# Kernel tuning notes

Measured on AMD Instinct MI355X. Metric: run time of the kernel, lower is better.

Reference implementation:

```python
import jax, jax.numpy as jnp
import numpy as np

SIZE = 1024
M = 10            # log2(SIZE); number of butterfly factors
N_TERMS = 10
BATCH = 8192

# diagonal offset of butterfly j (order matches torch: range(m)[::-1])
DIAGS = [1 << (M - 1 - j) for j in range(M)]


def setup_inputs() -> dict:
    key = jax.random.key(0)
    k1, k2, k3, k4, k5 = jax.random.split(key, 5)
    x = jax.random.normal(k1, (BATCH, SIZE), dtype=jnp.float32)
    diag = jax.random.normal(k2, (M, SIZE), dtype=jnp.float32)
    subpad = jax.random.normal(k3, (M, SIZE), dtype=jnp.float32)
    suppad = jax.random.normal(k4, (M, SIZE), dtype=jnp.float32)
    logit = jax.random.normal(k5, (N_TERMS, M), dtype=jnp.float32)
    # zero the padded positions: subdiag has length SIZE-d stored in [d:],
    # superdiag has length SIZE-d stored in [:-d]
    idx = np.arange(SIZE)
    sub_mask = np.stack([idx >= d for d in DIAGS]).astype(np.float32)
    sup_mask = np.stack([idx < SIZE - d for d in DIAGS]).astype(np.float32)
    subpad = subpad * jnp.asarray(sub_mask)
    suppad = suppad * jnp.asarray(sup_mask)
    return {"x": x, "diag": diag, "subpad": subpad, "suppad": suppad, "logit": logit}


def _butterfly(x, dg, sb, sp, d):
    # out = dg*x; out[d:] += subdiag*x[:-d]; out[:-d] += superdiag*x[d:]
    z = jnp.zeros(x.shape[:-1] + (d,), x.dtype)
    x_right = jnp.concatenate([z, x[..., :-d]], axis=-1)  # x shifted right by d
    x_left = jnp.concatenate([x[..., d:], z], axis=-1)    # x shifted left by d
    return dg * x + sb * x_right + sp * x_left


def reference(x, diag, subpad, suppad, logit):
    prob = jax.nn.softmax(logit, axis=-1)  # (n_terms, m)
    out = x
    for i in range(N_TERMS)[::-1]:
        # apply all m butterflies to current output, stack on last dim
        ys = jnp.stack(
            [_butterfly(out, diag[j], subpad[j], suppad[j], DIAGS[j]) for j in range(M)],
            axis=-1,
        )  # (..., size, m)
        out = jnp.einsum('bsm,m->bs', ys, prob[i])
    return out
```

## Files before the change

kernel.cpp:

```cpp
#include <hip/hip_runtime.h>

#define SIZE 1024
#define MM 10
#define NTERMS 10

typedef _Float16 f16;
typedef __attribute__((ext_vector_type(8))) _Float16 f16x8;
typedef __attribute__((ext_vector_type(4))) _Float16 f16x4;
typedef __attribute__((ext_vector_type(4))) float    f32x4;
typedef __attribute__((ext_vector_type(2))) int      i2;

typedef const __attribute__((address_space(1))) _Float16 gf16;
typedef __attribute__((address_space(3))) _Float16 sf16;

__device__ __forceinline__ float4 ldq(const float* p) { return *(const float4*)p; }

#define FMA4F(W, v0, v1, v2, v3)                                     \
    a0 = fmaf((W)[0], (v0), a0); a1 = fmaf((W)[1], (v1), a1);        \
    a2 = fmaf((W)[2], (v2), a2); a3 = fmaf((W)[3], (v3), a3);

__device__ __forceinline__ void cvt16(const float4& v0, const float4& v1, f16x8& h) {
    h[0] = (f16)v0.x; h[1] = (f16)v0.y; h[2] = (f16)v0.z; h[3] = (f16)v0.w;
    h[4] = (f16)v1.x; h[5] = (f16)v1.y; h[6] = (f16)v1.z; h[7] = (f16)v1.w;
}

__global__ __launch_bounds__(256)
void cvt_x(const float* __restrict__ x, f16* __restrict__ xh)
{
    const long i = ((long)blockIdx.x * 256 + threadIdx.x) * 16;
    const float4 a = ldq(x + i), b = ldq(x + i + 4),
                 c = ldq(x + i + 8), d = ldq(x + i + 12);
    f16x8 h0, h1; cvt16(a, b, h0); cvt16(c, d, h1);
    *(f16x8*)(xh + i)     = h0;
    *(f16x8*)(xh + i + 8) = h1;
}

__global__ __launch_bounds__(256, 2)
void precompute_G(const float* __restrict__ diag,
                  const float* __restrict__ subpad,
                  const float* __restrict__ suppad,
                  const float* __restrict__ logit,
                  float* __restrict__ G)
{
    __shared__ float buf[2][2][SIZE];

    const int tid = threadIdx.x;
    const int s0  = tid * 4;
    const int rowbase = blockIdx.x * 2;

    #pragma unroll
    for (int r = 0; r < 2; ++r) {
        float4 v;
        v.x = (rowbase + r == s0 + 0) ? 1.f : 0.f;
        v.y = (rowbase + r == s0 + 1) ? 1.f : 0.f;
        v.z = (rowbase + r == s0 + 2) ? 1.f : 0.f;
        v.w = (rowbase + r == s0 + 3) ? 1.f : 0.f;
        *(float4*)&buf[0][r][s0] = v;
    }
    __syncthreads();

    int cur = 0;
    for (int t = 0; t < NTERMS; ++t) {
        const int i = NTERMS - 1 - t;

        float lg[MM];
        float mx = -3.4e38f;
        #pragma unroll
        for (int j = 0; j < MM; ++j) { lg[j] = logit[i * MM + j]; mx = fmaxf(mx, lg[j]); }
        float ssum = 0.f;
        #pragma unroll
        for (int j = 0; j < MM; ++j) { lg[j] = __expf(lg[j] - mx); ssum += lg[j]; }
        const float inv = 1.0f / ssum;

        float D[4] = {0.f, 0.f, 0.f, 0.f};
        float Wsb[MM][4], Wsp[MM][4];
        #pragma unroll
        for (int j = 0; j < MM; ++j) {
            const float pj = lg[j] * inv;
            const float4 dg = ldq(diag   + j * SIZE + s0);
            const float4 sb = ldq(subpad + j * SIZE + s0);
            const float4 sp = ldq(suppad + j * SIZE + s0);
            D[0] = fmaf(pj, dg.x, D[0]); D[1] = fmaf(pj, dg.y, D[1]);
            D[2] = fmaf(pj, dg.z, D[2]); D[3] = fmaf(pj, dg.w, D[3]);
            Wsb[j][0] = pj * sb.x; Wsb[j][1] = pj * sb.y;
            Wsb[j][2] = pj * sb.z; Wsb[j][3] = pj * sb.w;
            Wsp[j][0] = pj * sp.x; Wsp[j][1] = pj * sp.y;
            Wsp[j][2] = pj * sp.z; Wsp[j][3] = pj * sp.w;
        }

        const bool last = (t == NTERMS - 1);
        for (int r = 0; r < 2; ++r) {
            const float* row = &buf[cur][r][0];

            const float4 xo = ldq(row + s0);
            float a0 = D[0] * xo.x, a1 = D[1] * xo.y,
                  a2 = D[2] * xo.z, a3 = D[3] * xo.w;

            const float4 xl = ldq(row + (s0 >= 4         ? s0 - 4 : 0));
            const float4 xr = ldq(row + (s0 + 4 <= 1020  ? s0 + 4 : 1020));

            FMA4F(Wsb[9], xl.w, xo.x, xo.y, xo.z)
            FMA4F(Wsp[9], xo.y, xo.z, xo.w, xr.x)
            FMA4F(Wsb[8], xl.z, xl.w, xo.x, xo.y)
            FMA4F(Wsp[8], xo.z, xo.w, xr.x, xr.y)
            FMA4F(Wsb[7], xl.x, xl.y, xl.z, xl.w)
            FMA4F(Wsp[7], xr.x, xr.y, xr.z, xr.w)
            #pragma unroll
            for (int j = 0; j <= 6; ++j) {
                const int d = 512 >> j;
                const float4 xm = ldq(row + (s0 >= d        ? s0 - d : 0));
                const float4 xp = ldq(row + (s0 + d <= 1020 ? s0 + d : 1020));
                FMA4F(Wsb[j], xm.x, xm.y, xm.z, xm.w)
                FMA4F(Wsp[j], xp.x, xp.y, xp.z, xp.w)
            }

            if (last) {
                *(float4*)(G + (long)(rowbase + r) * SIZE + s0) =
                    make_float4(a0, a1, a2, a3);
            } else {
                *(float4*)&buf[cur ^ 1][r][s0] = make_float4(a0, a1, a2, a3);
            }
        }
        __syncthreads();
        cur ^= 1;
    }
}

__global__ __launch_bounds__(256)
void transpose_cast(const float* __restrict__ G, f16* __restrict__ Gt)
{
    __shared__ float tile[64][65];
    const int tid = threadIdx.x;
    const int k0 = blockIdx.x * 64;
    const int s0 = blockIdx.y * 64;
    const int rr = tid >> 4;
    const int cc = (tid & 15) * 4;

    #pragma unroll
    for (int p = 0; p < 4; ++p) {
        const float4 v = ldq(G + (long)(k0 + rr + p * 16) * SIZE + s0 + cc);
        *(float4*)&tile[rr + p * 16][cc] = v;
    }
    __syncthreads();
    #pragma unroll
    for (int p = 0; p < 4; ++p) {
        const int s = rr + p * 16;
        f16x4 h;
        h[0] = (f16)tile[cc + 0][s];
        h[1] = (f16)tile[cc + 1][s];
        h[2] = (f16)tile[cc + 2][s];
        h[3] = (f16)tile[cc + 3][s];
        *(f16x4*)(Gt + (long)(s0 + s) * SIZE + k0 + cc) = h;
    }
}

#define BMT 128
#define BNT 128
#define BKT 32
#define NKT (1024 / BKT)

__global__ __launch_bounds__(256, 2)
void gemm_f16(const f16* __restrict__ xh,
              const f16* __restrict__ Gt,
              float* __restrict__ out)
{
    __shared__ f16 Xs[2][BMT][BKT];

    const int tid  = threadIdx.x;
    const int bm   = blockIdx.x & 63;
    const int bn   = blockIdx.x >> 6;
    const int w    = tid >> 6, lane = tid & 63;
    const int wm   = w >> 1,  wn   = w & 1;
    const int lr   = lane & 15, lk = lane >> 4;

    const f16* gsrc = xh + (long)(bm * BMT + (tid >> 2)) * 1024 + (tid & 3) * 8;

    const f16* gbase = Gt + (long)(bn * BNT + wn * 64 + lr) * 1024 + lk * 8;

    f32x4 acc[4][4];
    #pragma unroll
    for (int mi = 0; mi < 4; ++mi)
        #pragma unroll
        for (int ni = 0; ni < 4; ++ni)
            acc[mi][ni] = (f32x4){0.f, 0.f, 0.f, 0.f};

    f16x8 b0, b1, b2, b3;
    f16x8 c0, c1, c2, c3;

#define STAGE(BUF, KT) {                                                      \
        const f16* gp = gsrc + (KT) * BKT;                                    \
        sf16* lp = (sf16*)(&Xs[BUF][0][0] + (tid >> 6) * 512);                \
        __builtin_amdgcn_global_load_lds((gf16*)gp,              lp,       16, 0, 0); \
        __builtin_amdgcn_global_load_lds((gf16*)(gp + 64 * 1024), lp + 2048, 16, 0, 0); }
#define LOAD_B(B0, B1, B2, B3, KT) {                                  \
        const f16* gp = gbase + (KT) * BKT;                           \
        B0 = *(const f16x8*)(gp);                                     \
        B1 = *(const f16x8*)(gp + 16 * 1024);                         \
        B2 = *(const f16x8*)(gp + 32 * 1024);                         \
        B3 = *(const f16x8*)(gp + 48 * 1024); }
#define COMPUTE(BUF, B0, B1, B2, B3) {                                \
        f16x8 a0 = *(const f16x8*)&Xs[BUF][wm * 64 +  0 + lr][lk * 8];\
        f16x8 a1 = *(const f16x8*)&Xs[BUF][wm * 64 + 16 + lr][lk * 8];\
        f16x8 a2 = *(const f16x8*)&Xs[BUF][wm * 64 + 32 + lr][lk * 8];\
        f16x8 a3 = *(const f16x8*)&Xs[BUF][wm * 64 + 48 + lr][lk * 8];\
        acc[0][0] = __builtin_amdgcn_mfma_f32_16x16x32_f16(a0, B0, acc[0][0], 0, 0, 0); \
        acc[0][1] = __builtin_amdgcn_mfma_f32_16x16x32_f16(a0, B1, acc[0][1], 0, 0, 0); \
        acc[0][2] = __builtin_amdgcn_mfma_f32_16x16x32_f16(a0, B2, acc[0][2], 0, 0, 0); \
        acc[0][3] = __builtin_amdgcn_mfma_f32_16x16x32_f16(a0, B3, acc[0][3], 0, 0, 0); \
        acc[1][0] = __builtin_amdgcn_mfma_f32_16x16x32_f16(a1, B0, acc[1][0], 0, 0, 0); \
        acc[1][1] = __builtin_amdgcn_mfma_f32_16x16x32_f16(a1, B1, acc[1][1], 0, 0, 0); \
        acc[1][2] = __builtin_amdgcn_mfma_f32_16x16x32_f16(a1, B2, acc[1][2], 0, 0, 0); \
        acc[1][3] = __builtin_amdgcn_mfma_f32_16x16x32_f16(a1, B3, acc[1][3], 0, 0, 0); \
        acc[2][0] = __builtin_amdgcn_mfma_f32_16x16x32_f16(a2, B0, acc[2][0], 0, 0, 0); \
        acc[2][1] = __builtin_amdgcn_mfma_f32_16x16x32_f16(a2, B1, acc[2][1], 0, 0, 0); \
        acc[2][2] = __builtin_amdgcn_mfma_f32_16x16x32_f16(a2, B2, acc[2][2], 0, 0, 0); \
        acc[2][3] = __builtin_amdgcn_mfma_f32_16x16x32_f16(a2, B3, acc[2][3], 0, 0, 0); \
        acc[3][0] = __builtin_amdgcn_mfma_f32_16x16x32_f16(a3, B0, acc[3][0], 0, 0, 0); \
        acc[3][1] = __builtin_amdgcn_mfma_f32_16x16x32_f16(a3, B1, acc[3][1], 0, 0, 0); \
        acc[3][2] = __builtin_amdgcn_mfma_f32_16x16x32_f16(a3, B2, acc[3][2], 0, 0, 0); \
        acc[3][3] = __builtin_amdgcn_mfma_f32_16x16x32_f16(a3, B3, acc[3][3], 0, 0, 0); }

    STAGE(0, 0); LOAD_B(b0, b1, b2, b3, 0);
    __syncthreads();

    #pragma unroll 1
    for (int kt2 = 0; kt2 < NKT / 2; ++kt2) {
        const int kt = kt2 * 2;
        STAGE(1, kt + 1);
        LOAD_B(c0, c1, c2, c3, kt + 1);
        COMPUTE(0, b0, b1, b2, b3);
        __syncthreads();
        if (kt2 < NKT / 2 - 1) {
            STAGE(0, kt + 2);
            LOAD_B(b0, b1, b2, b3, kt + 2);
        }
        COMPUTE(1, c0, c1, c2, c3);
        __syncthreads();
    }

    const long orow0 = (long)bm * BMT + wm * 64 + lk * 4;
    const int  ocol0 = bn * BNT + wn * 64 + lr;
    #pragma unroll
    for (int mi = 0; mi < 4; ++mi)
        #pragma unroll
        for (int ni = 0; ni < 4; ++ni)
            #pragma unroll
            for (int q = 0; q < 4; ++q)
                out[(orow0 + mi * 16 + q) * 1024 + ocol0 + ni * 16] = acc[mi][ni][q];

#undef STAGE
#undef LOAD_B
#undef COMPUTE
}

#define RPB 16
#define MIX_L(acc, r32, ww) \
    asm("v_fma_mix_f32 %0, %1, %2, %0 op_sel:[0,0,0] op_sel_hi:[1,0,0]" \
        : "+v"(acc) : "v"(r32), "v"(ww))
#define MIX_H(acc, r32, ww) \
    asm("v_fma_mix_f32 %0, %1, %2, %0 op_sel:[1,0,0] op_sel_hi:[1,0,0]" \
        : "+v"(acc) : "v"(r32), "v"(ww))

__global__ __launch_bounds__(256, 2)
void butterfly_h16mix(const float* __restrict__ x,
                      const float* __restrict__ diag,
                      const float* __restrict__ subpad,
                      const float* __restrict__ suppad,
                      const float* __restrict__ logit,
                      float* __restrict__ out)
{
    __shared__ f16 buf[2][RPB][SIZE];
    const int tid = threadIdx.x;
    const int s0  = tid * 4;
    const long rowbase = (long)blockIdx.x * RPB;

    #pragma unroll
    for (int r = 0; r < RPB; ++r) {
        const float4 v = ldq(x + (rowbase + r) * SIZE + s0);
        f16x4 h;
        h[0] = (f16)v.x; h[1] = (f16)v.y; h[2] = (f16)v.z; h[3] = (f16)v.w;
        *(f16x4*)&buf[0][r][s0] = h;
    }
    __syncthreads();

    int cur = 0;
    for (int t = 0; t < NTERMS; ++t) {
        const int i = NTERMS - 1 - t;
        float lg[MM];
        float mx = -3.4e38f;
        #pragma unroll
        for (int j = 0; j < MM; ++j) { lg[j] = logit[i * MM + j]; mx = fmaxf(mx, lg[j]); }
        float ssum = 0.f;
        #pragma unroll
        for (int j = 0; j < MM; ++j) { lg[j] = __expf(lg[j] - mx); ssum += lg[j]; }
        const float inv = 1.0f / ssum;

        float D[4] = {0.f, 0.f, 0.f, 0.f};
        float Wsb[MM][4], Wsp[MM][4];
        #pragma unroll
        for (int j = 0; j < MM; ++j) {
            const float pj = lg[j] * inv;
            const float4 dg = ldq(diag   + j * SIZE + s0);
            const float4 sb = ldq(subpad + j * SIZE + s0);
            const float4 sp = ldq(suppad + j * SIZE + s0);
            D[0] = fmaf(pj, dg.x, D[0]); D[1] = fmaf(pj, dg.y, D[1]);
            D[2] = fmaf(pj, dg.z, D[2]); D[3] = fmaf(pj, dg.w, D[3]);
            Wsb[j][0] = pj * sb.x; Wsb[j][1] = pj * sb.y;
            Wsb[j][2] = pj * sb.z; Wsb[j][3] = pj * sb.w;
            Wsp[j][0] = pj * sp.x; Wsp[j][1] = pj * sp.y;
            Wsp[j][2] = pj * sp.z; Wsp[j][3] = pj * sp.w;
        }

        const bool last = (t == NTERMS - 1);
        for (int r = 0; r < RPB; ++r) {
            const f16* row = &buf[cur][r][0];
            const i2 xo = *(const i2*)&row[s0];
            const i2 xl = *(const i2*)&row[(s0 >= 4)        ? s0 - 4 : 0];
            const i2 xr = *(const i2*)&row[(s0 + 4 <= 1020) ? s0 + 4 : 1020];
            float a0 = 0.f, a1 = 0.f, a2 = 0.f, a3 = 0.f;

            MIX_L(a0, xo.x, D[0]); MIX_H(a1, xo.x, D[1]);
            MIX_L(a2, xo.y, D[2]); MIX_H(a3, xo.y, D[3]);
            MIX_H(a0, xl.y, Wsb[9][0]); MIX_L(a1, xo.x, Wsb[9][1]);
            MIX_H(a2, xo.x, Wsb[9][2]); MIX_L(a3, xo.y, Wsb[9][3]);
            MIX_H(a0, xo.x, Wsp[9][0]); MIX_L(a1, xo.y, Wsp[9][1]);
            MIX_H(a2, xo.y, Wsp[9][2]); MIX_L(a3, xr.x, Wsp[9][3]);
            MIX_L(a0, xl.y, Wsb[8][0]); MIX_H(a1, xl.y, Wsb[8][1]);
            MIX_L(a2, xo.x, Wsb[8][2]); MIX_H(a3, xo.x, Wsb[8][3]);
            MIX_L(a0, xo.y, Wsp[8][0]); MIX_H(a1, xo.y, Wsp[8][1]);
            MIX_L(a2, xr.x, Wsp[8][2]); MIX_H(a3, xr.x, Wsp[8][3]);
            MIX_L(a0, xl.x, Wsb[7][0]); MIX_H(a1, xl.x, Wsb[7][1]);
            MIX_L(a2, xl.y, Wsb[7][2]); MIX_H(a3, xl.y, Wsb[7][3]);
            MIX_L(a0, xr.x, Wsp[7][0]); MIX_H(a1, xr.x, Wsp[7][1]);
            MIX_L(a2, xr.y, Wsp[7][2]); MIX_H(a3, xr.y, Wsp[7][3]);
            #pragma unroll
            for (int j = 0; j <= 6; ++j) {
                const int d = 512 >> j;
                const i2 xm = *(const i2*)&row[(s0 >= d)        ? s0 - d : 0];
                const i2 xp = *(const i2*)&row[(s0 + d <= 1020) ? s0 + d : 1020];
                MIX_L(a0, xm.x, Wsb[j][0]); MIX_H(a1, xm.x, Wsb[j][1]);
                MIX_L(a2, xm.y, Wsb[j][2]); MIX_H(a3, xm.y, Wsb[j][3]);
                MIX_L(a0, xp.x, Wsp[j][0]); MIX_H(a1, xp.x, Wsp[j][1]);
                MIX_L(a2, xp.y, Wsp[j][2]); MIX_H(a3, xp.y, Wsp[j][3]);
            }

            if (last) {
                *(float4*)(out + (rowbase + r) * SIZE + s0) =
                    make_float4(a0, a1, a2, a3);
            } else {
                f16x4 hv;
                hv[0] = (f16)a0; hv[1] = (f16)a1; hv[2] = (f16)a2; hv[3] = (f16)a3;
                *(f16x4*)&buf[cur ^ 1][r][s0] = hv;
            }
        }
        __syncthreads();
        cur ^= 1;
    }
}

extern "C" void kernel_launch(void* const* d_in, const int* in_sizes, int n_in,
                              void* d_out, int out_size, void* d_ws, size_t ws_size,
                              hipStream_t stream) {
    const float* x      = (const float*)d_in[0];
    const float* diag   = (const float*)d_in[1];
    const float* subpad = (const float*)d_in[2];
    const float* suppad = (const float*)d_in[3];
    const float* logit  = (const float*)d_in[4];
    float* outp = (float*)d_out;

    const int batch = in_sizes[0] / SIZE;
    const size_t needG  = (size_t)SIZE * SIZE * sizeof(float);
    const size_t needGt = (size_t)SIZE * SIZE * sizeof(f16);
    const size_t needXh = (size_t)batch * SIZE * sizeof(f16);

    if (d_ws != nullptr && ws_size >= needG + needGt + needXh) {
        float* G  = (float*)d_ws;
        f16*   Gt = (f16*)((char*)d_ws + needG);
        f16*   xh = (f16*)((char*)d_ws + needG + needGt);
        precompute_G<<<dim3(SIZE / 2), dim3(256), 0, stream>>>(
            diag, subpad, suppad, logit, G);
        transpose_cast<<<dim3(16, 16), dim3(256), 0, stream>>>(G, Gt);
        cvt_x<<<dim3((int)(((long)batch * SIZE) / (256 * 16))), dim3(256), 0, stream>>>(x, xh);
        const int nblocks = (batch / BMT) * (SIZE / BNT);
        gemm_f16<<<dim3(nblocks), dim3(256), 0, stream>>>(xh, Gt, outp);
    } else {
        butterfly_h16mix<<<dim3(batch / RPB), dim3(256), 0, stream>>>(
            x, diag, subpad, suppad, logit, outp);
    }
}
```

Measured before the change: 87.39 us.

## Fuse G precompute, transpose-cast and x conversion; use single-wave 64x64 GEMM tiles

Merges precompute_G, transpose_cast and cvt_x into one launch. Extra blocks handle the x-to-f16 conversion, and the G rows are written straight into transposed f16 Gt with scalar strided stores, so the fp32 G buffer and its reread go away. The GEMM is recut from 256-thread 128x128 tiles into 64-thread single-wave 64x64 tiles, giving four times as many blocks. This removes two launches and an intermediate round trip, at the cost of uncoalesced transposed stores and less data reuse per block in the GEMM.

```diff
diff --git a/kernel.cpp b/kernel.cpp
--- a/kernel.cpp
+++ b/kernel.cpp
@@ -24,27 +24,29 @@
     h[4] = (f16)v1.x; h[5] = (f16)v1.y; h[6] = (f16)v1.z; h[7] = (f16)v1.w;
 }
 
-__global__ __launch_bounds__(256)
-void cvt_x(const float* __restrict__ x, f16* __restrict__ xh)
-{
-    const long i = ((long)blockIdx.x * 256 + threadIdx.x) * 16;
-    const float4 a = ldq(x + i), b = ldq(x + i + 4),
-                 c = ldq(x + i + 8), d = ldq(x + i + 12);
-    f16x8 h0, h1; cvt16(a, b, h0); cvt16(c, d, h1);
-    *(f16x8*)(xh + i)     = h0;
-    *(f16x8*)(xh + i + 8) = h1;
-}
-
 __global__ __launch_bounds__(256, 2)
-void precompute_G(const float* __restrict__ diag,
-                  const float* __restrict__ subpad,
-                  const float* __restrict__ suppad,
-                  const float* __restrict__ logit,
-                  float* __restrict__ G)
+void fused_pre(const float* __restrict__ x,
+               const float* __restrict__ diag,
+               const float* __restrict__ subpad,
+               const float* __restrict__ suppad,
+               const float* __restrict__ logit,
+               f16* __restrict__ Gt,
+               f16* __restrict__ xh)
 {
     __shared__ float buf[2][2][SIZE];
 
     const int tid = threadIdx.x;
+
+    if (blockIdx.x >= 512) {
+        const long i = ((long)(blockIdx.x - 512) * 256 + tid) * 16;
+        const float4 a = ldq(x + i), b = ldq(x + i + 4),
+                     c = ldq(x + i + 8), d = ldq(x + i + 12);
+        f16x8 h0, h1; cvt16(a, b, h0); cvt16(c, d, h1);
+        *(f16x8*)(xh + i)     = h0;
+        *(f16x8*)(xh + i + 8) = h1;
+        return;
+    }
+
     const int s0  = tid * 4;
     const int rowbase = blockIdx.x * 2;
 
@@ -115,8 +117,11 @@
             }
 
             if (last) {
-                *(float4*)(G + (long)(rowbase + r) * SIZE + s0) =
-                    make_float4(a0, a1, a2, a3);
+                const int k = rowbase + r;
+                Gt[(long)(s0 + 0) * SIZE + k] = (f16)a0;
+                Gt[(long)(s0 + 1) * SIZE + k] = (f16)a1;
+                Gt[(long)(s0 + 2) * SIZE + k] = (f16)a2;
+                Gt[(long)(s0 + 3) * SIZE + k] = (f16)a3;
             } else {
                 *(float4*)&buf[cur ^ 1][r][s0] = make_float4(a0, a1, a2, a3);
             }
@@ -126,56 +131,23 @@
     }
 }
 
-__global__ __launch_bounds__(256)
-void transpose_cast(const float* __restrict__ G, f16* __restrict__ Gt)
+#define NKT 32
+
+__global__ __launch_bounds__(64)
+void gemm64(const f16* __restrict__ xh,
+            const f16* __restrict__ Gt,
+            float* __restrict__ out)
 {
-    __shared__ float tile[64][65];
-    const int tid = threadIdx.x;
-    const int k0 = blockIdx.x * 64;
-    const int s0 = blockIdx.y * 64;
-    const int rr = tid >> 4;
-    const int cc = (tid & 15) * 4;
-
-    #pragma unroll
-    for (int p = 0; p < 4; ++p) {
-        const float4 v = ldq(G + (long)(k0 + rr + p * 16) * SIZE + s0 + cc);
-        *(float4*)&tile[rr + p * 16][cc] = v;
-    }
-    __syncthreads();
-    #pragma unroll
-    for (int p = 0; p < 4; ++p) {
-        const int s = rr + p * 16;
-        f16x4 h;
-        h[0] = (f16)tile[cc + 0][s];
-        h[1] = (f16)tile[cc + 1][s];
-        h[2] = (f16)tile[cc + 2][s];
-        h[3] = (f16)tile[cc + 3][s];
-        *(f16x4*)(Gt + (long)(s0 + s) * SIZE + k0 + cc) = h;
-    }
-}
-
-#define BMT 128
-#define BNT 128
-#define BKT 32
-#define NKT (1024 / BKT)
-
-__global__ __launch_bounds__(256, 2)
-void gemm_f16(const f16* __restrict__ xh,
-              const f16* __restrict__ Gt,
-              float* __restrict__ out)
-{
-    __shared__ f16 Xs[2][BMT][BKT];
-
-    const int tid  = threadIdx.x;
-    const int bm   = blockIdx.x & 63;
-    const int bn   = blockIdx.x >> 6;
-    const int w    = tid >> 6, lane = tid & 63;
-    const int wm   = w >> 1,  wn   = w & 1;
+    __shared__ f16 Xs[2][64][32];
+
+    const int lane = threadIdx.x;
+    const int bm   = blockIdx.x & 127;
+    const int bn   = blockIdx.x >> 7;
     const int lr   = lane & 15, lk = lane >> 4;
 
-    const f16* gsrc = xh + (long)(bm * BMT + (tid >> 2)) * 1024 + (tid & 3) * 8;
-
-    const f16* gbase = Gt + (long)(bn * BNT + wn * 64 + lr) * 1024 + lk * 8;
+    const f16* gsrc = xh + (long)(bm * 64 + (lane >> 2)) * 1024 + (lane & 3) * 8;
+
+    const f16* gbase = Gt + (long)(bn * 64 + lr) * 1024 + lk * 8;
 
     f32x4 acc[4][4];
     #pragma unroll
@@ -188,21 +160,23 @@
     f16x8 c0, c1, c2, c3;
 
 #define STAGE(BUF, KT) {                                                      \
-        const f16* gp = gsrc + (KT) * BKT;                                    \
-        sf16* lp = (sf16*)(&Xs[BUF][0][0] + (tid >> 6) * 512);                \
-        __builtin_amdgcn_global_load_lds((gf16*)gp,              lp,       16, 0, 0); \
-        __builtin_amdgcn_global_load_lds((gf16*)(gp + 64 * 1024), lp + 2048, 16, 0, 0); }
+        const f16* gp = gsrc + (KT) * 32;                                     \
+        sf16* lp = (sf16*)&Xs[BUF][0][0];                                     \
+        __builtin_amdgcn_global_load_lds((gf16*)gp,               lp,        16, 0, 0); \
+        __builtin_amdgcn_global_load_lds((gf16*)(gp + 16 * 1024), lp +  512, 16, 0, 0); \
+        __builtin_amdgcn_global_load_lds((gf16*)(gp + 32 * 1024), lp + 1024, 16, 0, 0); \
+        __builtin_amdgcn_global_load_lds((gf16*)(gp + 48 * 1024), lp + 1536, 16, 0, 0); }
 #define LOAD_B(B0, B1, B2, B3, KT) {                                  \
-        const f16* gp = gbase + (KT) * BKT;                           \
+        const f16* gp = gbase + (KT) * 32;                            \
         B0 = *(const f16x8*)(gp);                                     \
         B1 = *(const f16x8*)(gp + 16 * 1024);                         \
         B2 = *(const f16x8*)(gp + 32 * 1024);                         \
         B3 = *(const f16x8*)(gp + 48 * 1024); }
 #define COMPUTE(BUF, B0, B1, B2, B3) {                                \
-        f16x8 a0 = *(const f16x8*)&Xs[BUF][wm * 64 +  0 + lr][lk * 8];\
-        f16x8 a1 = *(const f16x8*)&Xs[BUF][wm * 64 + 16 + lr][lk * 8];\
-        f16x8 a2 = *(const f16x8*)&Xs[BUF][wm * 64 + 32 + lr][lk * 8];\
-        f16x8 a3 = *(const f16x8*)&Xs[BUF][wm * 64 + 48 + lr][lk * 8];\
+        f16x8 a0 = *(const f16x8*)&Xs[BUF][ 0 + lr][lk * 8];          \
+        f16x8 a1 = *(const f16x8*)&Xs[BUF][16 + lr][lk * 8];          \
+        f16x8 a2 = *(const f16x8*)&Xs[BUF][32 + lr][lk * 8];          \
+        f16x8 a3 = *(const f16x8*)&Xs[BUF][48 + lr][lk * 8];          \
         acc[0][0] = __builtin_amdgcn_mfma_f32_16x16x32_f16(a0, B0, acc[0][0], 0, 0, 0); \
         acc[0][1] = __builtin_amdgcn_mfma_f32_16x16x32_f16(a0, B1, acc[0][1], 0, 0, 0); \
         acc[0][2] = __builtin_amdgcn_mfma_f32_16x16x32_f16(a0, B2, acc[0][2], 0, 0, 0); \
@@ -238,8 +212,8 @@
         __syncthreads();
     }
 
-    const long orow0 = (long)bm * BMT + wm * 64 + lk * 4;
-    const int  ocol0 = bn * BNT + wn * 64 + lr;
+    const long orow0 = (long)bm * 64 + lk * 4;
+    const int  ocol0 = bn * 64 + lr;
     #pragma unroll
     for (int mi = 0; mi < 4; ++mi)
         #pragma unroll
@@ -369,20 +343,17 @@
     float* outp = (float*)d_out;
 
     const int batch = in_sizes[0] / SIZE;
-    const size_t needG  = (size_t)SIZE * SIZE * sizeof(float);
     const size_t needGt = (size_t)SIZE * SIZE * sizeof(f16);
     const size_t needXh = (size_t)batch * SIZE * sizeof(f16);
 
-    if (d_ws != nullptr && ws_size >= needG + needGt + needXh) {
-        float* G  = (float*)d_ws;
-        f16*   Gt = (f16*)((char*)d_ws + needG);
-        f16*   xh = (f16*)((char*)d_ws + needG + needGt);
-        precompute_G<<<dim3(SIZE / 2), dim3(256), 0, stream>>>(
-            diag, subpad, suppad, logit, G);
-        transpose_cast<<<dim3(16, 16), dim3(256), 0, stream>>>(G, Gt);
-        cvt_x<<<dim3((int)(((long)batch * SIZE) / (256 * 16))), dim3(256), 0, stream>>>(x, xh);
-        const int nblocks = (batch / BMT) * (SIZE / BNT);
-        gemm_f16<<<dim3(nblocks), dim3(256), 0, stream>>>(xh, Gt, outp);
+    if (d_ws != nullptr && ws_size >= needGt + needXh) {
+        f16* Gt = (f16*)d_ws;
+        f16* xh = (f16*)((char*)d_ws + needGt);
+        const int cvtBlocks = (int)(((long)batch * SIZE) / (256 * 16));
+        fused_pre<<<dim3(512 + cvtBlocks), dim3(256), 0, stream>>>(
+            x, diag, subpad, suppad, logit, Gt, xh);
+        const int nblocks = (batch / 64) * (SIZE / 64);
+        gemm64<<<dim3(nblocks), dim3(64), 0, stream>>>(xh, Gt, outp);
     } else {
         butterfly_h16mix<<<dim3(batch / RPB), dim3(256), 0, stream>>>(
             x, diag, subpad, suppad, logit, outp);
```

New measurement: 82.03 us. -6.1%, faster.
